# Optimization experiments

Hardware: AMD Instinct MI355X
Metric: run time of the kernel (lower is better)

## Reference

```python
import jax, jax.numpy as jnp
import numpy as np

KERNEL_BW = 0.4  # RBF (Laplacian) kernel bandwidth from the original code


def setup_inputs() -> dict:
    key = jax.random.key(0)
    k1, k2 = jax.random.split(key)
    N, C = 8192, 1000
    inp = jax.random.normal(k1, (N, C), dtype=jnp.float32)
    target = jax.random.randint(k2, (N,), 0, C, dtype=jnp.int64)
    return {"input": inp, "target": target}


def reference(input, target):
    # input: [N, C] logits; target: [N] int labels
    target = target.reshape(-1)
    probs = jax.nn.softmax(input, axis=1)
    predicted_probs = jnp.max(probs, axis=1)           # [N] confidence p_i
    pred_labels = jnp.argmax(probs, axis=1)            # [N]
    correct_mask = (pred_labels == target).astype(predicted_probs.dtype)  # [N]
    c_minus_r = correct_mask - predicted_probs          # [N]
    # Pairwise terms: dot[i,j] = (c_i - p_i)(c_j - p_j); k[i,j] = exp(-|p_i - p_j| / 0.4)
    dot_product = jnp.outer(c_minus_r, c_minus_r)       # [N, N]
    kernel = jnp.exp(-jnp.abs(predicted_probs[:, None] - predicted_probs[None, :]) / KERNEL_BW)
    n = predicted_probs.shape[0]
    return jnp.sum(dot_product * kernel) / jnp.asarray(n, predicted_probs.dtype) ** 2
```

## Files before the change

kernel.cpp:

```cpp
#include <hip/hip_runtime.h>
#include <math.h>
#include <stdint.h>


#define WAVE 64
static constexpr float KBW_INV = 2.5f;

__global__ __launch_bounds__(256) void rowstats_kernel(
    const float* __restrict__ inp, const int* __restrict__ tgt,
    float2* __restrict__ AB, unsigned long long* __restrict__ acc,
    unsigned int* __restrict__ counter, int N, int C) {
  if (blockIdx.x == 0 && threadIdx.x == 0) { *acc = 0ull; *counter = 0u; }
  const int wave = threadIdx.x >> 6;
  const int lane = threadIdx.x & 63;
  const int row = blockIdx.x * 4 + wave;
  if (row >= N) return;
  const int C4 = C >> 2;
  const float4* rp = reinterpret_cast<const float4*>(inp + (size_t)row * C);

  float4 x[4];
  bool valid[4];
  float m = -INFINITY;
  int am = 0x7fffffff;
  #pragma unroll
  for (int w = 0; w < 4; ++w) {
    const int k = lane + w * WAVE;
    valid[w] = (k < C4);
    if (valid[w]) {
      float4 v = rp[k];
      x[w] = v;
      const int base = k * 4;
      if (v.x > m) { m = v.x; am = base + 0; }
      if (v.y > m) { m = v.y; am = base + 1; }
      if (v.z > m) { m = v.z; am = base + 2; }
      if (v.w > m) { m = v.w; am = base + 3; }
    }
  }
  #pragma unroll
  for (int off = 32; off; off >>= 1) {
    float om = __shfl_xor(m, off);
    int oi = __shfl_xor(am, off);
    if (om > m || (om == m && oi < am)) { m = om; am = oi; }
  }
  float s = 0.f;
  #pragma unroll
  for (int w = 0; w < 4; ++w) {
    if (valid[w]) {
      s += __expf(x[w].x - m) + __expf(x[w].y - m) +
           __expf(x[w].z - m) + __expf(x[w].w - m);
    }
  }
  #pragma unroll
  for (int off = 32; off; off >>= 1) s += __shfl_xor(s, off);

  if (lane == 0) {
    const float p = 1.0f / s;
    const float v = ((tgt[row] == am) ? 1.0f : 0.0f) - p;
    float2 ab;
    ab.x = v * __expf(-p * KBW_INV);
    ab.y = v * __expf(p * KBW_INV);
    AB[row] = ab;
  }
}

#define IPT 4
#define JBLK 128

static constexpr double FXSCALE = 1073741824.0;

__global__ __launch_bounds__(256) void pairwise_kernel(
    const float2* __restrict__ AB, unsigned long long* __restrict__ acc,
    unsigned int* __restrict__ counter, float* __restrict__ out, int N,
    int nBlocks) {
  __shared__ float2 sj[JBLK];
  const int nJB = N / JBLK;
  const int bi = blockIdx.x / nJB;
  const int bj = blockIdx.x % nJB;
  const int tid = threadIdx.x;

  if (tid < JBLK) sj[tid] = AB[bj * JBLK + tid];

  float2 abi[IPT];
  #pragma unroll
  for (int u = 0; u < IPT; ++u) abi[u] = AB[bi * (256 * IPT) + u * 256 + tid];
  __syncthreads();

  float facc[IPT];
  #pragma unroll
  for (int u = 0; u < IPT; ++u) facc[u] = 0.f;

  #pragma unroll 8
  for (int t = 0; t < JBLK; ++t) {
    const float aj = sj[t].x;
    const float bj_ = sj[t].y;
    #pragma unroll
    for (int u = 0; u < IPT; ++u) {
      const float xx = abi[u].x * bj_;
      const float yy = abi[u].y * aj;
      facc[u] += __builtin_amdgcn_fmed3f(xx, yy, 0.0f);
    }
  }

  double dacc = (double)((facc[0] + facc[1]) + (facc[2] + facc[3]));
  #pragma unroll
  for (int off = 32; off; off >>= 1) dacc += __shfl_xor(dacc, off);
  __shared__ double wsum[4];
  if ((tid & 63) == 0) wsum[tid >> 6] = dacc;
  __syncthreads();
  if (tid == 0) {
    const double blocksum = (wsum[0] + wsum[1]) + (wsum[2] + wsum[3]);
    const long long fx = __double2ll_rn(blocksum * FXSCALE);
    atomicAdd(acc, (unsigned long long)fx);
    __threadfence();
    const unsigned int done = atomicAdd(counter, 1u);
    if (done == (unsigned int)nBlocks - 1u) {
      const unsigned long long total = atomicAdd(acc, 0ull);
      const double s = (double)(long long)total * (1.0 / FXSCALE);
      out[0] = (float)(s / ((double)N * (double)N));
    }
  }
}

extern "C" void kernel_launch(void* const* d_in, const int* in_sizes, int n_in,
                              void* d_out, int out_size, void* d_ws, size_t ws_size,
                              hipStream_t stream) {
  const float* inp = (const float*)d_in[0];
  const int* tgt = (const int*)d_in[1];
  const int N = in_sizes[1];
  const int C = in_sizes[0] / N;

  float2* AB = (float2*)d_ws;
  unsigned long long* acc =
      (unsigned long long*)(((uintptr_t)(AB + N) + 15) & ~(uintptr_t)15);
  unsigned int* counter = (unsigned int*)(acc + 1);

  const int rowBlocks = (N + 3) / 4;
  rowstats_kernel<<<rowBlocks, 256, 0, stream>>>(inp, tgt, AB, acc, counter, N, C);

  const int nIB = N / (256 * IPT);
  const int nJB = N / JBLK;
  const int nPair = nIB * nJB;
  pairwise_kernel<<<nPair, 256, 0, stream>>>(AB, acc, counter, (float*)d_out,
                                             N, nPair);
}
```

Baseline: 30.55 us.

## Fuse row-stats and pairwise kernels into one cooperative kernel with grid sync

Merges the softmax row-statistics pass and the pairwise reduction into a single cooperative kernel, separated by a grid-wide sync instead of a second launch. Each wave now handles four rows at once with all loads issued up front, giving more memory-level parallelism, and out-of-range columns are padded with -inf instead of using validity flags. The aim is to remove the inter-kernel launch gap and the tail of the first kernel. In exchange it pays the cost of a grid barrier, and the launch only works if all 512 blocks fit on the device at the same time.

```diff
diff --git a/kernel.cpp b/kernel.cpp
--- a/kernel.cpp
+++ b/kernel.cpp
@@ -1,88 +1,111 @@
 #include <hip/hip_runtime.h>
+#include <hip/hip_cooperative_groups.h>
 #include <math.h>
 #include <stdint.h>
 
+namespace cg = cooperative_groups;
 
-#define WAVE 64
+
 static constexpr float KBW_INV = 2.5f;
+static constexpr double FXSCALE = 1073741824.0;
 
-__global__ __launch_bounds__(256) void rowstats_kernel(
+#define TPB 256
+#define RPW 4
+#define JBLK 128
+#define IPT 4
+
+__global__ __launch_bounds__(TPB) void mmce_fused(
     const float* __restrict__ inp, const int* __restrict__ tgt,
     float2* __restrict__ AB, unsigned long long* __restrict__ acc,
-    unsigned int* __restrict__ counter, int N, int C) {
-  if (blockIdx.x == 0 && threadIdx.x == 0) { *acc = 0ull; *counter = 0u; }
-  const int wave = threadIdx.x >> 6;
-  const int lane = threadIdx.x & 63;
-  const int row = blockIdx.x * 4 + wave;
-  if (row >= N) return;
+    unsigned int* __restrict__ counter, float* __restrict__ out,
+    int N, int C, int nJB, int nBlocks) {
+  const int tid = threadIdx.x;
+  const int wv = tid >> 6;
+  const int lane = tid & 63;
+
+  if (blockIdx.x == 0 && tid == 0) { *acc = 0ull; *counter = 0u; }
+
   const int C4 = C >> 2;
-  const float4* rp = reinterpret_cast<const float4*>(inp + (size_t)row * C);
+  const int rowbase = blockIdx.x * (4 * RPW) + wv * RPW;
 
-  float4 x[4];
-  bool valid[4];
-  float m = -INFINITY;
-  int am = 0x7fffffff;
+  float4 x[RPW][4];
   #pragma unroll
-  for (int w = 0; w < 4; ++w) {
-    const int k = lane + w * WAVE;
-    valid[w] = (k < C4);
-    if (valid[w]) {
-      float4 v = rp[k];
-      x[w] = v;
-      const int base = k * 4;
-      if (v.x > m) { m = v.x; am = base + 0; }
-      if (v.y > m) { m = v.y; am = base + 1; }
-      if (v.z > m) { m = v.z; am = base + 2; }
-      if (v.w > m) { m = v.w; am = base + 3; }
+  for (int r = 0; r < RPW; ++r) {
+    const float4* rp =
+        reinterpret_cast<const float4*>(inp + (size_t)(rowbase + r) * C);
+    #pragma unroll
+    for (int w = 0; w < 4; ++w) {
+      const int k = lane + w * 64;
+      x[r][w] = (k < C4)
+                    ? rp[k]
+                    : make_float4(-INFINITY, -INFINITY, -INFINITY, -INFINITY);
+    }
+  }
+
+  float m[RPW];
+  int am[RPW];
+  #pragma unroll
+  for (int r = 0; r < RPW; ++r) {
+    m[r] = -INFINITY;
+    am[r] = 0x7fffffff;
+    #pragma unroll
+    for (int w = 0; w < 4; ++w) {
+      const int base = (lane + w * 64) * 4;
+      const float4 v = x[r][w];
+      if (v.x > m[r]) { m[r] = v.x; am[r] = base + 0; }
+      if (v.y > m[r]) { m[r] = v.y; am[r] = base + 1; }
+      if (v.z > m[r]) { m[r] = v.z; am[r] = base + 2; }
+      if (v.w > m[r]) { m[r] = v.w; am[r] = base + 3; }
     }
   }
   #pragma unroll
   for (int off = 32; off; off >>= 1) {
-    float om = __shfl_xor(m, off);
-    int oi = __shfl_xor(am, off);
-    if (om > m || (om == m && oi < am)) { m = om; am = oi; }
+    #pragma unroll
+    for (int r = 0; r < RPW; ++r) {
+      const float om = __shfl_xor(m[r], off);
+      const int oi = __shfl_xor(am[r], off);
+      if (om > m[r] || (om == m[r] && oi < am[r])) { m[r] = om; am[r] = oi; }
+    }
   }
-  float s = 0.f;
+  float s[RPW];
   #pragma unroll
-  for (int w = 0; w < 4; ++w) {
-    if (valid[w]) {
-      s += __expf(x[w].x - m) + __expf(x[w].y - m) +
-           __expf(x[w].z - m) + __expf(x[w].w - m);
+  for (int r = 0; r < RPW; ++r) {
+    s[r] = 0.f;
+    #pragma unroll
+    for (int w = 0; w < 4; ++w) {
+      s[r] += __expf(x[r][w].x - m[r]) + __expf(x[r][w].y - m[r]) +
+              __expf(x[r][w].z - m[r]) + __expf(x[r][w].w - m[r]);
     }
   }
   #pragma unroll
-  for (int off = 32; off; off >>= 1) s += __shfl_xor(s, off);
+  for (int off = 32; off; off >>= 1) {
+    #pragma unroll
+    for (int r = 0; r < RPW; ++r) s[r] += __shfl_xor(s[r], off);
+  }
+  if (lane == 0) {
+    #pragma unroll
+    for (int r = 0; r < RPW; ++r) {
+      const float p = 1.0f / s[r];
+      const float v = ((tgt[rowbase + r] == am[r]) ? 1.0f : 0.0f) - p;
+      float2 ab;
+      ab.x = v * __expf(-p * KBW_INV);
+      ab.y = v * __expf(p * KBW_INV);
+      AB[rowbase + r] = ab;
+    }
+  }
 
-  if (lane == 0) {
-    const float p = 1.0f / s;
-    const float v = ((tgt[row] == am) ? 1.0f : 0.0f) - p;
-    float2 ab;
-    ab.x = v * __expf(-p * KBW_INV);
-    ab.y = v * __expf(p * KBW_INV);
-    AB[row] = ab;
-  }
-}
+  cg::this_grid().sync();
 
-#define IPT 4
-#define JBLK 128
-
-static constexpr double FXSCALE = 1073741824.0;
-
-__global__ __launch_bounds__(256) void pairwise_kernel(
-    const float2* __restrict__ AB, unsigned long long* __restrict__ acc,
-    unsigned int* __restrict__ counter, float* __restrict__ out, int N,
-    int nBlocks) {
   __shared__ float2 sj[JBLK];
-  const int nJB = N / JBLK;
   const int bi = blockIdx.x / nJB;
   const int bj = blockIdx.x % nJB;
-  const int tid = threadIdx.x;
 
   if (tid < JBLK) sj[tid] = AB[bj * JBLK + tid];
 
   float2 abi[IPT];
   #pragma unroll
-  for (int u = 0; u < IPT; ++u) abi[u] = AB[bi * (256 * IPT) + u * 256 + tid];
+  for (int u = 0; u < IPT; ++u)
+    abi[u] = AB[bi * (TPB * IPT) + u * TPB + tid];
   __syncthreads();
 
   float facc[IPT];
@@ -115,8 +138,8 @@
     const unsigned int done = atomicAdd(counter, 1u);
     if (done == (unsigned int)nBlocks - 1u) {
       const unsigned long long total = atomicAdd(acc, 0ull);
-      const double s = (double)(long long)total * (1.0 / FXSCALE);
-      out[0] = (float)(s / ((double)N * (double)N));
+      const double sum = (double)(long long)total * (1.0 / FXSCALE);
+      out[0] = (float)(sum / ((double)N * (double)N));
     }
   }
 }
@@ -126,20 +149,19 @@
                               hipStream_t stream) {
   const float* inp = (const float*)d_in[0];
   const int* tgt = (const int*)d_in[1];
-  const int N = in_sizes[1];
-  const int C = in_sizes[0] / N;
+  int N = in_sizes[1];
+  int C = in_sizes[0] / N;
 
   float2* AB = (float2*)d_ws;
   unsigned long long* acc =
       (unsigned long long*)(((uintptr_t)(AB + N) + 15) & ~(uintptr_t)15);
   unsigned int* counter = (unsigned int*)(acc + 1);
+  float* out = (float*)d_out;
 
-  const int rowBlocks = (N + 3) / 4;
-  rowstats_kernel<<<rowBlocks, 256, 0, stream>>>(inp, tgt, AB, acc, counter, N, C);
+  int nBlocks = N / (4 * RPW);
+  int nJB = N / JBLK;
 
-  const int nIB = N / (256 * IPT);
-  const int nJB = N / JBLK;
-  const int nPair = nIB * nJB;
-  pairwise_kernel<<<nPair, 256, 0, stream>>>(AB, acc, counter, (float*)d_out,
-                                             N, nPair);
+  void* args[] = {&inp, &tgt, &AB, &acc, &counter, &out, &N, &C, &nJB, &nBlocks};
+  hipLaunchCooperativeKernel((const void*)mmce_fused, dim3(nBlocks), dim3(TPB),
+                             args, 0, stream);
 }
```

Result: slower. 78.60 us (+157.3%).
